# Performance work log

Hardware: AMD Instinct MI355X
Metric: run time of the kernel (lower is better)

The kernel has to match this reference:

```python
import jax, jax.numpy as jnp
import numpy as np

DIM = 1024
DIM_INNER = 2048
B, S = 4, 4096


def setup_inputs() -> dict:
    key = jax.random.key(0)
    k1, k2, k3 = jax.random.split(key, 3)
    x = jax.random.normal(k1, (B, S, DIM), dtype=jnp.float32)
    # torch Linear weight init ~ U(-1/sqrt(fan_in), 1/sqrt(fan_in)); scaled normals are fine
    W_hg = jax.random.normal(k2, (DIM, 2 * DIM_INNER), dtype=jnp.float32) / np.sqrt(DIM)
    W_out = jax.random.normal(k3, (DIM_INNER, DIM), dtype=jnp.float32) / np.sqrt(DIM_INNER)
    return {"x": x, "W_hg": W_hg, "W_out": W_out}


def heinsen_associative_scan_log(log_coeffs, log_values):
    # a_star[t] = sum_{i<=t} log_coeffs[i]
    a_star = jnp.cumsum(log_coeffs, axis=1)
    log_h0_plus_b_star = jax.lax.cumlogsumexp(log_values - a_star, axis=1)
    return jnp.exp(a_star + log_h0_plus_b_star)


def reference(x, W_hg, W_out):
    # fused projection then split into hidden / gate, each [B, S, DIM_INNER]
    hg = jnp.einsum('bsd,de->bse', x, W_hg)
    hidden, gate = jnp.split(hg, 2, axis=-1)
    # seq_len > 1, prev_hidden = None path of the torch module
    log_z = jax.nn.log_sigmoid(gate)                 # log sigmoid(gate)
    log_coeffs = -jax.nn.softplus(gate)              # log(1 - sigmoid(gate))
    hidden_log = jnp.log(jax.nn.relu(hidden) + 0.5)  # log(g(hidden)) as coded (relu+0.5)
    log_values = hidden_log + log_z
    h = heinsen_associative_scan_log(log_coeffs, log_values)  # [B, S, DIM_INNER]
    out = jnp.einsum('bse,ed->bsd', h, W_out)
    return out
```

## Files before the change

### kernel.cpp

```cpp
#include <hip/hip_runtime.h>
#include <stdint.h>

#define DIMX 1024
#define DIM_INNER 2048
#define BATCH 4
#define SEQ 4096
#define M_TOTAL (BATCH * SEQ)
#define N_HG (2 * DIM_INNER)
#define NCHUNK 32
#define CLEN 128

typedef unsigned short u16;
typedef __attribute__((ext_vector_type(8))) short short8;
typedef __attribute__((ext_vector_type(4))) float floatx4;

__device__ __forceinline__ float bflo(uint32_t u) { return __uint_as_float(u << 16); }
__device__ __forceinline__ float bfhi(uint32_t u) { return __uint_as_float(u & 0xffff0000u); }
__device__ __forceinline__ uint32_t f2bf_bits(float f) {
    uint32_t u = __float_as_uint(f);
    return (u + 0x7fffu + ((u >> 16) & 1u)) >> 16;
}

__global__ __launch_bounds__(256) void prep(const float* __restrict__ x,
                                            const float* __restrict__ Whg,
                                            const float* __restrict__ Wout,
                                            u16* __restrict__ xb,
                                            u16* __restrict__ whgt,
                                            u16* __restrict__ woutt) {
    __shared__ float tile[64][65];
    const int bid = blockIdx.x;
    const int tid = threadIdx.x;
    if (bid < 2048) {
        const int n4 = M_TOTAL * DIMX / 4;
        const float4* in4 = (const float4*)x;
        ushort4* out4 = (ushort4*)xb;
        for (int i = bid * 256 + tid; i < n4; i += 2048 * 256) {
            float4 v = in4[i];
            ushort4 o;
            o.x = (u16)f2bf_bits(v.x);
            o.y = (u16)f2bf_bits(v.y);
            o.z = (u16)f2bf_bits(v.z);
            o.w = (u16)f2bf_bits(v.w);
            out4[i] = o;
        }
        return;
    }
    const float* in;
    u16* out;
    int R, C, tb;
    if (bid < 3072) {
        in = Whg; out = whgt; R = DIMX; C = N_HG; tb = bid - 2048;
    } else {
        in = Wout; out = woutt; R = DIM_INNER; C = DIMX; tb = bid - 3072;
    }
    const int tilesx = C / 64;
    const int c0 = (tb % tilesx) * 64, r0 = (tb / tilesx) * 64;
    const int tx = tid & 63, ty = tid >> 6;
#pragma unroll
    for (int i = ty; i < 64; i += 4)
        tile[i][tx] = in[(size_t)(r0 + i) * C + c0 + tx];
    __syncthreads();
#pragma unroll
    for (int i = ty; i < 64; i += 4)
        out[(size_t)(c0 + i) * R + r0 + tx] = (u16)f2bf_bits(tile[tx][i]);
}

__global__ __launch_bounds__(256, 2) void gemm1_k(const u16* __restrict__ A,
                                                  const u16* __restrict__ Bt,
                                                  uint32_t* __restrict__ av,
                                                  float2* __restrict__ sumAV) {
    __shared__ alignas(16) char smem[65536];
    u16* As = (u16*)smem;
    u16* Bh = (u16*)(smem + 8192);
    u16* Bg = (u16*)(smem + 16384);
    uint32_t* avl = (uint32_t*)smem;

    const int tid = threadIdx.x;
    const int lane = tid & 63;
    const int wave = tid >> 6;
    const int wm = (wave >> 1) * 64;
    const int wn = (wave & 1) * 64;
    const size_t m0 = (size_t)blockIdx.y * 128;
    const int n0 = blockIdx.x * 128;

    floatx4 acch[4][4], accg[4][4];
#pragma unroll
    for (int i = 0; i < 4; ++i)
#pragma unroll
        for (int j = 0; j < 4; ++j) {
            acch[i][j] = (floatx4){0.f, 0.f, 0.f, 0.f};
            accg[i][j] = (floatx4){0.f, 0.f, 0.f, 0.f};
        }

    const int srow = lane >> 2;
    const int scol = ((lane & 3) ^ ((srow >> 1) & 3)) * 8;
    const u16* Ag = A + m0 * DIMX + (size_t)(wave * 16 + srow) * DIMX + scol;
    const u16* Bhg = Bt + (size_t)n0 * DIMX + (size_t)(wave * 16 + srow) * DIMX + scol;
    const u16* Bgg = Bt + (size_t)(DIM_INNER + n0) * DIMX + (size_t)(wave * 16 + srow) * DIMX + scol;
    u16* Asw = As + (wave * 16) * 32;
    u16* Bhw = Bh + (wave * 16) * 32;
    u16* Bgw = Bg + (wave * 16) * 32;

    const int fr = lane & 15;
    const int kblk = lane >> 4;
    const int koff = (kblk ^ ((fr >> 1) & 3)) * 8;

    for (int k0 = 0; k0 < DIMX; k0 += 32) {
        __syncthreads();
#pragma unroll
        for (int i = 0; i < 2; ++i) {
            __builtin_amdgcn_global_load_lds(
                (const __attribute__((address_space(1))) uint32_t*)(const void*)(Ag + (size_t)i * 64 * DIMX + k0),
                (__attribute__((address_space(3))) uint32_t*)(void*)(Asw + i * 64 * 32), 16, 0, 0);
            __builtin_amdgcn_global_load_lds(
                (const __attribute__((address_space(1))) uint32_t*)(const void*)(Bhg + (size_t)i * 64 * DIMX + k0),
                (__attribute__((address_space(3))) uint32_t*)(void*)(Bhw + i * 64 * 32), 16, 0, 0);
            __builtin_amdgcn_global_load_lds(
                (const __attribute__((address_space(1))) uint32_t*)(const void*)(Bgg + (size_t)i * 64 * DIMX + k0),
                (__attribute__((address_space(3))) uint32_t*)(void*)(Bgw + i * 64 * 32), 16, 0, 0);
        }
        __syncthreads();

        short8 af[4], bhf[4], bgf[4];
#pragma unroll
        for (int i = 0; i < 4; ++i)
            af[i] = *(const short8*)(As + (wm + i * 16 + fr) * 32 + koff);
#pragma unroll
        for (int j = 0; j < 4; ++j) {
            bhf[j] = *(const short8*)(Bh + (wn + j * 16 + fr) * 32 + koff);
            bgf[j] = *(const short8*)(Bg + (wn + j * 16 + fr) * 32 + koff);
        }
#pragma unroll
        for (int i = 0; i < 4; ++i)
#pragma unroll
            for (int j = 0; j < 4; ++j) {
                acch[i][j] = __builtin_amdgcn_mfma_f32_16x16x32_bf16(af[i], bhf[j], acch[i][j], 0, 0, 0);
                accg[i][j] = __builtin_amdgcn_mfma_f32_16x16x32_bf16(af[i], bgf[j], accg[i][j], 0, 0, 0);
            }
    }
    __syncthreads();

    const int r0row = (lane >> 4) * 4;
#pragma unroll
    for (int i = 0; i < 4; ++i) {
#pragma unroll
        for (int r = 0; r < 4; ++r) {
            const int row = wm + i * 16 + r0row + r;
#pragma unroll
            for (int j = 0; j < 4; ++j) {
                const int col = wn + j * 16 + fr;
                float h = acch[i][j][r];
                float g = accg[i][j][r];
                g = fminf(fmaxf(g, -30.f), 30.f);
                float e = __expf(-g);
                float z = 1.f / (1.f + e);
                float a = e * z;
                float v = z * (fmaxf(h, 0.f) + 0.5f);
                uint32_t pk = f2bf_bits(a) | (f2bf_bits(v) << 16);
                avl[row * 128 + col] = pk;
                av[(m0 + row) * 2048 + n0 + col] = pk;
            }
        }
    }
    __syncthreads();

    const int col = tid & 127;
    const int rlo = (tid >> 7) * 64;
    float Aa = 1.f, Vv = 0.f;
#pragma unroll 8
    for (int j = 0; j < 64; ++j) {
        uint32_t pk = avl[(rlo + j) * 128 + col];
        float a = bflo(pk), v = bfhi(pk);
        Vv = fmaf(a, Vv, v);
        Aa *= a;
    }
    __syncthreads();
    if (tid < 128) {
        avl[col] = __float_as_uint(Aa);
        avl[128 + col] = __float_as_uint(Vv);
    }
    __syncthreads();
    if (tid >= 128) {
        float Al = __uint_as_float(avl[col]);
        float Vl = __uint_as_float(avl[128 + col]);
        float At = Al * Aa;
        float Vt = fmaf(Aa, Vl, Vv);
        const int chunk = (int)(m0 >> 7);
        sumAV[(size_t)chunk * 2048 + n0 + col] = (float2){At, Vt};
    }
}

__global__ __launch_bounds__(256, 2) void gemm2_k(const u16* __restrict__ A,
                                                  const u16* __restrict__ Bt,
                                                  float* __restrict__ C) {
    const int M = M_TOTAL, N = DIMX, K = DIM_INNER;
    __shared__ alignas(16) u16 As[128 * 32];
    __shared__ alignas(16) u16 Bs[128 * 32];

    const int tid = threadIdx.x;
    const int lane = tid & 63;
    const int wave = tid >> 6;
    const int wm = (wave >> 1) * 64;
    const int wn = (wave & 1) * 64;
    const size_t m0 = (size_t)blockIdx.y * 128;
    const size_t n0 = (size_t)blockIdx.x * 128;

    floatx4 acc[4][4];
#pragma unroll
    for (int i = 0; i < 4; ++i)
#pragma unroll
        for (int j = 0; j < 4; ++j) acc[i][j] = (floatx4){0.f, 0.f, 0.f, 0.f};

    const int srow = lane >> 2;
    const int scol = ((lane & 3) ^ ((srow >> 1) & 3)) * 8;
    const u16* Ag = A + m0 * K + (size_t)(wave * 16 + srow) * K + scol;
    const u16* Bg = Bt + n0 * K + (size_t)(wave * 16 + srow) * K + scol;
    u16* Asw = As + (wave * 16) * 32;
    u16* Bsw = Bs + (wave * 16) * 32;

    const int fr = lane & 15;
    const int kblk = lane >> 4;
    const int koff = (kblk ^ ((fr >> 1) & 3)) * 8;

    for (int k0 = 0; k0 < K; k0 += 32) {
        __syncthreads();
#pragma unroll
        for (int i = 0; i < 2; ++i) {
            __builtin_amdgcn_global_load_lds(
                (const __attribute__((address_space(1))) uint32_t*)(const void*)(Ag + (size_t)i * 64 * K + k0),
                (__attribute__((address_space(3))) uint32_t*)(void*)(Asw + i * 64 * 32), 16, 0, 0);
            __builtin_amdgcn_global_load_lds(
                (const __attribute__((address_space(1))) uint32_t*)(const void*)(Bg + (size_t)i * 64 * K + k0),
                (__attribute__((address_space(3))) uint32_t*)(void*)(Bsw + i * 64 * 32), 16, 0, 0);
        }
        __syncthreads();

        short8 af[4], bfr[4];
#pragma unroll
        for (int i = 0; i < 4; ++i)
            af[i] = *(const short8*)(As + (wm + i * 16 + fr) * 32 + koff);
#pragma unroll
        for (int j = 0; j < 4; ++j)
            bfr[j] = *(const short8*)(Bs + (wn + j * 16 + fr) * 32 + koff);
#pragma unroll
        for (int i = 0; i < 4; ++i)
#pragma unroll
            for (int j = 0; j < 4; ++j)
                acc[i][j] = __builtin_amdgcn_mfma_f32_16x16x32_bf16(af[i], bfr[j], acc[i][j], 0, 0, 0);
    }

    const int r0row = (lane >> 4) * 4;
#pragma unroll
    for (int i = 0; i < 4; ++i)
#pragma unroll
        for (int r = 0; r < 4; ++r) {
            size_t row = m0 + wm + i * 16 + r0row + r;
#pragma unroll
            for (int j = 0; j < 4; ++j) {
                size_t col = n0 + wn + j * 16 + fr;
                C[row * N + col] = acc[i][j][r];
            }
        }
}

__global__ __launch_bounds__(64) void scan_carry(const float2* __restrict__ sumAV,
                                                 float* __restrict__ carry) {
    const int g = blockIdx.x * 64 + threadIdx.x;
    const int b = g >> 11, c = g & 2047;
    float h = 0.f;
#pragma unroll 8
    for (int ch = 0; ch < NCHUNK; ++ch) {
        float2 s = sumAV[(size_t)(b * NCHUNK + ch) * 2048 + c];
        carry[(size_t)(b * NCHUNK + ch) * 2048 + c] = h;
        h = fmaf(s.x, h, s.y);
    }
}

__global__ __launch_bounds__(256) void scan_apply(const uint32_t* __restrict__ av,
                                                  const float* __restrict__ carry,
                                                  uint32_t* __restrict__ hbuf) {
    const int b = blockIdx.z, ch = blockIdx.y;
    const int c2 = blockIdx.x * 256 + threadIdx.x;
    const size_t rowbase = (size_t)b * SEQ + (size_t)ch * CLEN;
    const uint32_t* p = av + rowbase * 2048 + c2 * 2;
    uint32_t* q = hbuf + rowbase * 1024 + c2;
    const float2 cin = ((const float2*)carry)[(size_t)(b * NCHUNK + ch) * 1024 + c2];
    float h0 = cin.x, h1 = cin.y;
    uint2 p0 = *(const uint2*)(p);
    uint2 p1 = *(const uint2*)(p + 2048);
#pragma unroll 4
    for (int j = 0; j < CLEN; ++j) {
        uint2 p2;
        if (j + 2 < CLEN) p2 = *(const uint2*)(p + (size_t)(j + 2) * 2048);
        float a0 = bflo(p0.x), v0 = bfhi(p0.x);
        float a1 = bflo(p0.y), v1 = bfhi(p0.y);
        h0 = fmaf(a0, h0, v0);
        h1 = fmaf(a1, h1, v1);
        q[(size_t)j * 1024] = f2bf_bits(h0) | (f2bf_bits(h1) << 16);
        p0 = p1;
        p1 = p2;
    }
}

extern "C" void kernel_launch(void* const* d_in, const int* in_sizes, int n_in,
                              void* d_out, int out_size, void* d_ws, size_t ws_size,
                              hipStream_t stream) {
    const float* x = (const float*)d_in[0];
    const float* Whg = (const float*)d_in[1];
    const float* Wout = (const float*)d_in[2];

    char* ws = (char*)d_ws;
    size_t off = 0;
    u16* xb = (u16*)(ws + off);        off += (size_t)M_TOTAL * DIMX * 2;
    u16* whgt = (u16*)(ws + off);      off += (size_t)N_HG * DIMX * 2;
    u16* woutt = (u16*)(ws + off);     off += (size_t)DIMX * DIM_INNER * 2;
    uint32_t* av = (uint32_t*)(ws + off); off += (size_t)M_TOTAL * DIM_INNER * 4;
    uint32_t* hbuf = (uint32_t*)(ws + off); off += (size_t)M_TOTAL * DIM_INNER * 2;
    float2* sumAV = (float2*)(ws + off); off += (size_t)BATCH * NCHUNK * DIM_INNER * 8;
    float* carry = (float*)whgt;

    prep<<<2048 + 1024 + 512, 256, 0, stream>>>(x, Whg, Wout, xb, whgt, woutt);

    gemm1_k<<<dim3(16, 128), 256, 0, stream>>>(xb, whgt, av, sumAV);

    scan_carry<<<128, 64, 0, stream>>>(sumAV, carry);
    scan_apply<<<dim3(4, NCHUNK, BATCH), 256, 0, stream>>>(av, carry, hbuf);

    gemm2_k<<<dim3(8, 128), 256, 0, stream>>>((const u16*)hbuf, woutt, (float*)d_out);
}
```

Baseline: 421.9 us.

## Enlarge gemm2 block tile to 256x128 and deepen scan_apply prefetch

gemm2 now computes a 256x128 output tile per block: each wave owns 64 rows across all 128 columns, with 32 accumulators per wave, which raises the MFMA-to-LDS-load ratio and halves the number of blocks. scan_apply changes from a two-deep to a four-deep software prefetch, loading four rows per step to hide more global-load latency. The trade-off is higher register pressure in gemm2 under launch_bounds(256,2), fewer blocks (512) and therefore coarser load balance across CUs.

```diff
diff --git a/kernel.cpp b/kernel.cpp
--- a/kernel.cpp
+++ b/kernel.cpp
@@ -193,28 +193,27 @@
 __global__ __launch_bounds__(256, 2) void gemm2_k(const u16* __restrict__ A,
                                                   const u16* __restrict__ Bt,
                                                   float* __restrict__ C) {
-    const int M = M_TOTAL, N = DIMX, K = DIM_INNER;
-    __shared__ alignas(16) u16 As[128 * 32];
+    const int N = DIMX, K = DIM_INNER;
+    __shared__ alignas(16) u16 As[256 * 32];
     __shared__ alignas(16) u16 Bs[128 * 32];
 
     const int tid = threadIdx.x;
     const int lane = tid & 63;
     const int wave = tid >> 6;
-    const int wm = (wave >> 1) * 64;
-    const int wn = (wave & 1) * 64;
-    const size_t m0 = (size_t)blockIdx.y * 128;
+    const int wm = wave * 64;
+    const size_t m0 = (size_t)blockIdx.y * 256;
     const size_t n0 = (size_t)blockIdx.x * 128;
 
-    floatx4 acc[4][4];
+    floatx4 acc[4][8];
 #pragma unroll
     for (int i = 0; i < 4; ++i)
 #pragma unroll
-        for (int j = 0; j < 4; ++j) acc[i][j] = (floatx4){0.f, 0.f, 0.f, 0.f};
+        for (int j = 0; j < 8; ++j) acc[i][j] = (floatx4){0.f, 0.f, 0.f, 0.f};
 
     const int srow = lane >> 2;
     const int scol = ((lane & 3) ^ ((srow >> 1) & 3)) * 8;
-    const u16* Ag = A + m0 * K + (size_t)(wave * 16 + srow) * K + scol;
-    const u16* Bg = Bt + n0 * K + (size_t)(wave * 16 + srow) * K + scol;
+    const u16* Ag = A + (m0 + wave * 16 + srow) * K + scol;
+    const u16* Bg = Bt + (n0 + wave * 16 + srow) * K + scol;
     u16* Asw = As + (wave * 16) * 32;
     u16* Bsw = Bs + (wave * 16) * 32;
 
@@ -225,28 +224,29 @@
     for (int k0 = 0; k0 < K; k0 += 32) {
         __syncthreads();
 #pragma unroll
-        for (int i = 0; i < 2; ++i) {
+        for (int i = 0; i < 4; ++i)
             __builtin_amdgcn_global_load_lds(
                 (const __attribute__((address_space(1))) uint32_t*)(const void*)(Ag + (size_t)i * 64 * K + k0),
                 (__attribute__((address_space(3))) uint32_t*)(void*)(Asw + i * 64 * 32), 16, 0, 0);
+#pragma unroll
+        for (int i = 0; i < 2; ++i)
             __builtin_amdgcn_global_load_lds(
                 (const __attribute__((address_space(1))) uint32_t*)(const void*)(Bg + (size_t)i * 64 * K + k0),
                 (__attribute__((address_space(3))) uint32_t*)(void*)(Bsw + i * 64 * 32), 16, 0, 0);
-        }
         __syncthreads();
 
-        short8 af[4], bfr[4];
+        short8 af[4], bf[8];
 #pragma unroll
         for (int i = 0; i < 4; ++i)
             af[i] = *(const short8*)(As + (wm + i * 16 + fr) * 32 + koff);
 #pragma unroll
-        for (int j = 0; j < 4; ++j)
-            bfr[j] = *(const short8*)(Bs + (wn + j * 16 + fr) * 32 + koff);
-#pragma unroll
-        for (int i = 0; i < 4; ++i)
-#pragma unroll
-            for (int j = 0; j < 4; ++j)
-                acc[i][j] = __builtin_amdgcn_mfma_f32_16x16x32_bf16(af[i], bfr[j], acc[i][j], 0, 0, 0);
+        for (int j = 0; j < 8; ++j)
+            bf[j] = *(const short8*)(Bs + (j * 16 + fr) * 32 + koff);
+#pragma unroll
+        for (int i = 0; i < 4; ++i)
+#pragma unroll
+            for (int j = 0; j < 8; ++j)
+                acc[i][j] = __builtin_amdgcn_mfma_f32_16x16x32_bf16(af[i], bf[j], acc[i][j], 0, 0, 0);
     }
 
     const int r0row = (lane >> 4) * 4;
@@ -256,8 +256,8 @@
         for (int r = 0; r < 4; ++r) {
             size_t row = m0 + wm + i * 16 + r0row + r;
 #pragma unroll
-            for (int j = 0; j < 4; ++j) {
-                size_t col = n0 + wn + j * 16 + fr;
+            for (int j = 0; j < 8; ++j) {
+                size_t col = n0 + j * 16 + fr;
                 C[row * N + col] = acc[i][j][r];
             }
         }
@@ -286,19 +286,28 @@
     uint32_t* q = hbuf + rowbase * 1024 + c2;
     const float2 cin = ((const float2*)carry)[(size_t)(b * NCHUNK + ch) * 1024 + c2];
     float h0 = cin.x, h1 = cin.y;
-    uint2 p0 = *(const uint2*)(p);
-    uint2 p1 = *(const uint2*)(p + 2048);
-#pragma unroll 4
-    for (int j = 0; j < CLEN; ++j) {
-        uint2 p2;
-        if (j + 2 < CLEN) p2 = *(const uint2*)(p + (size_t)(j + 2) * 2048);
-        float a0 = bflo(p0.x), v0 = bfhi(p0.x);
-        float a1 = bflo(p0.y), v1 = bfhi(p0.y);
-        h0 = fmaf(a0, h0, v0);
-        h1 = fmaf(a1, h1, v1);
-        q[(size_t)j * 1024] = f2bf_bits(h0) | (f2bf_bits(h1) << 16);
-        p0 = p1;
-        p1 = p2;
+
+    uint2 buf[4];
+#pragma unroll
+    for (int t = 0; t < 4; ++t) buf[t] = *(const uint2*)(p + (size_t)t * 2048);
+
+    for (int j0 = 0; j0 < CLEN; j0 += 4) {
+        uint2 nxt[4];
+        if (j0 + 4 < CLEN) {
+#pragma unroll
+            for (int t = 0; t < 4; ++t)
+                nxt[t] = *(const uint2*)(p + (size_t)(j0 + 4 + t) * 2048);
+        }
+#pragma unroll
+        for (int t = 0; t < 4; ++t) {
+            float a0 = bflo(buf[t].x), v0 = bfhi(buf[t].x);
+            float a1 = bflo(buf[t].y), v1 = bfhi(buf[t].y);
+            h0 = fmaf(a0, h0, v0);
+            h1 = fmaf(a1, h1, v1);
+            q[(size_t)(j0 + t) * 1024] = f2bf_bits(h0) | (f2bf_bits(h1) << 16);
+        }
+#pragma unroll
+        for (int t = 0; t < 4; ++t) buf[t] = nxt[t];
     }
 }
 
@@ -326,5 +335,5 @@
     scan_carry<<<128, 64, 0, stream>>>(sumAV, carry);
     scan_apply<<<dim3(4, NCHUNK, BATCH), 256, 0, stream>>>(av, carry, hbuf);
 
-    gemm2_k<<<dim3(8, 128), 256, 0, stream>>>((const u16*)hbuf, woutt, (float*)d_out);
-}
+    gemm2_k<<<dim3(DIMX / 128, M_TOTAL / 256), 256, 0, stream>>>((const u16*)hbuf, woutt, (float*)d_out);
+}
```

New measurement: 417.2 us. Within noise of the previous version (-1.1%).
